# Kernel optimization log

Hardware: AMD Instinct MI355X
Metric: run time of the kernel (lower is better)

Reference implementation:

```python
import jax, jax.numpy as jnp
import numpy as np

B, S, H = 2, 1024, 1024
NH, HD = 16, 64
W = 4  # attention_window / number of cached previous-layer states
LS_INIT = 0.1  # layer_scale_init_value
EPS = 1e-5


def _layernorm(x, scale, bias):
    mu = jnp.mean(x, axis=-1, keepdims=True)
    var = jnp.mean(jnp.square(x - mu), axis=-1, keepdims=True)
    return (x - mu) * jax.lax.rsqrt(var + EPS) * scale + bias


def _rope(x, pos):
    # x: [B, L, NH, HD], pos: [L]
    half = x.shape[-1] // 2
    freq = 1.0 / (10000.0 ** (jnp.arange(half, dtype=x.dtype) / half))
    ang = pos.astype(x.dtype)[:, None] * freq[None, :]           # [L, half]
    cos = jnp.cos(ang)[None, :, None, :]
    sin = jnp.sin(ang)[None, :, None, :]
    x1, x2 = jnp.split(x, 2, axis=-1)
    return jnp.concatenate([x1 * cos - x2 * sin, x1 * sin + x2 * cos], axis=-1)


def setup_inputs() -> dict:
    key = jax.random.key(0)
    ks = jax.random.split(key, 8)
    w_std = 0.02
    return {
        'hidden_states': jax.random.normal(ks[0], (B, S, H), jnp.float32),
        'cache_states': jax.random.normal(ks[1], (W, B, S, H), jnp.float32),
        'ln_scale': jnp.ones((H,), jnp.float32),
        'ln_bias': jnp.zeros((H,), jnp.float32),
        'Wq': jax.random.normal(ks[2], (H, NH * HD), jnp.float32) * w_std,
        'Wk': jax.random.normal(ks[3], (H, NH * HD), jnp.float32) * w_std,
        'Wv': jax.random.normal(ks[4], (H, NH * HD), jnp.float32) * w_std,
        'Wo': jax.random.normal(ks[5], (NH * HD, H), jnp.float32) * w_std,
        'gate_param': jax.random.normal(ks[6], (H,), jnp.float32),
        'layer_scale_param': jnp.full((H,), LS_INIT, jnp.float32),
    }


def reference(hidden_states, cache_states, ln_scale, ln_bias, Wq, Wk, Wv, Wo,
              gate_param, layer_scale_param):
    b, s, h = hidden_states.shape
    w = cache_states.shape[0]

    # pre-norm
    normed = _layernorm(hidden_states, ln_scale, ln_bias)

    # gather cached previous-layer states (already normalized in cache) and
    # stack them with the current layer along the KV axis: [B, (W+1)*S, H]
    prev_flat = jnp.transpose(cache_states, (1, 0, 2, 3)).reshape(b, w * s, h)
    kv_in = jnp.concatenate([prev_flat, normed], axis=1)

    q = (normed @ Wq).reshape(b, s, NH, HD)
    k = (kv_in @ Wk).reshape(b, (w + 1) * s, NH, HD)
    v = (kv_in @ Wv).reshape(b, (w + 1) * s, NH, HD)

    pos_q = jnp.arange(s)
    pos_k = jnp.tile(jnp.arange(s), w + 1)  # same token positions per layer
    q = _rope(q, pos_q)
    k = _rope(k, pos_k)

    scale = 1.0 / jnp.sqrt(jnp.asarray(HD, hidden_states.dtype))
    scores = jnp.einsum('bqhd,bkhd->bhqk', q, k) * scale   # [B,NH,S,(W+1)S]
    attn = jax.nn.softmax(scores, axis=-1)
    ctx = jnp.einsum('bhqk,bkhd->bqhd', attn, v).reshape(b, s, NH * HD)
    attn_out = ctx @ Wo

    # gated residual with layer scale; cross_layer = most recent cached state
    cross_layer = cache_states[-1]
    g = jax.nn.sigmoid(gate_param)
    combined = g * attn_out + (1.0 - g) * cross_layer
    output = hidden_states + layer_scale_param * combined

    # LRU cache update: evict oldest slot, append normalized new state
    new_state = _layernorm(output, ln_scale, ln_bias)
    new_cache = jnp.concatenate([cache_states[1:], new_state[None]], axis=0)
    return output, new_cache
```

## Files before the change

### kernel.cpp

```cpp
#include <hip/hip_runtime.h>
#include <math.h>

typedef unsigned short u16;

constexpr int cB = 2;
constexpr int cS = 1024;
constexpr int cH = 1024;
constexpr int cNH = 16;
constexpr int cHD = 64;
constexpr int cW = 4;
constexpr int cL = (cW + 1) * cS;
constexpr float cEPS = 1e-5f;

typedef short s16x8 __attribute__((ext_vector_type(8)));
typedef float f32x4 __attribute__((ext_vector_type(4)));

__device__ __forceinline__ float u2f(u16 u) {
  union { unsigned int i; float f; } x; x.i = ((unsigned int)u) << 16; return x.f;
}
__device__ __forceinline__ u16 f2u(float f) {
  union { float f; unsigned int i; } x; x.f = f;
  unsigned int i = x.i;
  i += 0x7fffu + ((i >> 16) & 1u);
  return (u16)(i >> 16);
}
__device__ __forceinline__ u16 f2u_rt(float f) {
  union { __bf16 b; u16 u; } c; c.b = (__bf16)f; return c.u;
}
__device__ __forceinline__ s16x8 ld_frag(const u16* p) {
  uint4 v = *(const uint4*)p;
  union { uint4 u; s16x8 s; } c; c.u = v; return c.s;
}
__device__ __forceinline__ s16x8 u4_frag(uint4 v) {
  union { uint4 u; s16x8 s; } c; c.u = v; return c.s;
}
__device__ __forceinline__ void gl_lds16(const u16* g, u16* l) {
  __builtin_amdgcn_global_load_lds(
      (const __attribute__((address_space(1))) unsigned int*)g,
      (__attribute__((address_space(3))) unsigned int*)l, 16, 0, 0);
}
template <int CTRL>
__device__ __forceinline__ float dpp_fmax(float x) {
  union { float f; int i; } a, r;
  a.f = x;
  r.i = __builtin_amdgcn_update_dpp(a.i, a.i, CTRL, 0xF, 0xF, true);
  return fmaxf(x, r.f);
}

__global__ __launch_bounds__(256) void ln_f32(
    const float* __restrict__ src, float* __restrict__ dst,
    const float* __restrict__ scale, const float* __restrict__ bias)
{
  int r = blockIdx.x;
  int t = threadIdx.x;
  const float* sp = src + (size_t)r * cH;
  float4 x = ((const float4*)sp)[t];
  float s1 = x.x + x.y + x.z + x.w;
  float s2 = x.x * x.x + x.y * x.y + x.z * x.z + x.w * x.w;
  #pragma unroll
  for (int off = 32; off > 0; off >>= 1) {
    s1 += __shfl_down(s1, off);
    s2 += __shfl_down(s2, off);
  }
  __shared__ float w1[4], w2[4];
  __shared__ float stat[2];
  int wid = t >> 6, lid = t & 63;
  if (lid == 0) { w1[wid] = s1; w2[wid] = s2; }
  __syncthreads();
  if (t == 0) {
    float a = w1[0] + w1[1] + w1[2] + w1[3];
    float b = w2[0] + w2[1] + w2[2] + w2[3];
    float mu = a * (1.f / cH);
    float var = b * (1.f / cH) - mu * mu;
    if (var < 0.f) var = 0.f;
    stat[0] = mu; stat[1] = rsqrtf(var + cEPS);
  }
  __syncthreads();
  float mu = stat[0], rs = stat[1];
  int h0 = t * 4;
  float4 sc = *(const float4*)(scale + h0);
  float4 bi = *(const float4*)(bias + h0);
  float4 o;
  o.x = (x.x - mu) * rs * sc.x + bi.x;
  o.y = (x.y - mu) * rs * sc.y + bi.y;
  o.z = (x.z - mu) * rs * sc.z + bi.z;
  o.w = (x.w - mu) * rs * sc.w + bi.w;
  *(float4*)(dst + (size_t)r * cH + h0) = o;
}

__global__ __launch_bounds__(256) void ln_bf16(
    const float* __restrict__ src, u16* __restrict__ kvin,
    const float* __restrict__ scale, const float* __restrict__ bias)
{
  int r = blockIdx.x;
  int t = threadIdx.x;
  const float* sp = src + (size_t)r * cH;
  float4 x = ((const float4*)sp)[t];
  float s1 = x.x + x.y + x.z + x.w;
  float s2 = x.x * x.x + x.y * x.y + x.z * x.z + x.w * x.w;
  #pragma unroll
  for (int off = 32; off > 0; off >>= 1) {
    s1 += __shfl_down(s1, off);
    s2 += __shfl_down(s2, off);
  }
  __shared__ float w1[4], w2[4];
  __shared__ float stat[2];
  int wid = t >> 6, lid = t & 63;
  if (lid == 0) { w1[wid] = s1; w2[wid] = s2; }
  __syncthreads();
  if (t == 0) {
    float a = w1[0] + w1[1] + w1[2] + w1[3];
    float b = w2[0] + w2[1] + w2[2] + w2[3];
    float mu = a * (1.f / cH);
    float var = b * (1.f / cH) - mu * mu;
    if (var < 0.f) var = 0.f;
    stat[0] = mu; stat[1] = rsqrtf(var + cEPS);
  }
  __syncthreads();
  float mu = stat[0], rs = stat[1];
  int h0 = t * 4;
  float4 sc = *(const float4*)(scale + h0);
  float4 bi = *(const float4*)(bias + h0);
  int b = r >> 10, s = r & (cS - 1);
  u16* dp = kvin + ((size_t)(b * cL + cW * cS + s)) * cH + h0;
  ushort4 o; u16* op = (u16*)&o;
  op[0] = f2u((x.x - mu) * rs * sc.x + bi.x);
  op[1] = f2u((x.y - mu) * rs * sc.y + bi.y);
  op[2] = f2u((x.z - mu) * rs * sc.z + bi.z);
  op[3] = f2u((x.w - mu) * rs * sc.w + bi.w);
  *(ushort4*)dp = o;
}

__global__ __launch_bounds__(256) void cache2kv(const float* __restrict__ cache,
                                                u16* __restrict__ kvin) {
  int blk = blockIdx.x;
  int b = blk >> 12, w = (blk >> 10) & 3, s = blk & 1023;
  const float* src = cache + ((size_t)((w * cB + b) * cS + s)) * cH;
  u16* dst = kvin + ((size_t)(b * cL + w * cS + s)) * cH;
  int t = threadIdx.x;
  float4 v = *(const float4*)(src + t * 4);
  ushort4 o; u16* op = (u16*)&o;
  op[0] = f2u(v.x); op[1] = f2u(v.y); op[2] = f2u(v.z); op[3] = f2u(v.w);
  *(ushort4*)(dst + t * 4) = o;
}

__global__ __launch_bounds__(256) void wtrans(
    const float* __restrict__ W0, const float* __restrict__ W1,
    const float* __restrict__ W2, const float* __restrict__ W3,
    u16* __restrict__ Wt)
{
  __shared__ float tile[32][33];
  int mat = blockIdx.z;
  const float* W = (mat == 0) ? W0 : (mat == 1) ? W1 : (mat == 2) ? W2 : W3;
  u16* out = Wt + (size_t)mat * cH * cH;
  int k0 = blockIdx.y * 32, n0 = blockIdx.x * 32;
  int t = threadIdx.x;
  int r = t >> 3, c = (t & 7) * 4;
  float4 v = *(const float4*)(W + (size_t)(k0 + r) * cH + n0 + c);
  tile[r][c] = v.x; tile[r][c + 1] = v.y; tile[r][c + 2] = v.z; tile[r][c + 3] = v.w;
  __syncthreads();
  ushort4 o; u16* op = (u16*)&o;
  #pragma unroll
  for (int j = 0; j < 4; j++) op[j] = f2u(tile[c + j][r]);
  *(ushort4*)(out + (size_t)(n0 + r) * cH + k0 + c) = o;
}

constexpr int GBM = 128, GBN = 128, TLD = 136;

__global__ __launch_bounds__(256) void mgemm(
    const u16* __restrict__ A, const u16* __restrict__ Wt,
    int a_rpb, int a_base, int a_stride,
    int c_rpb, int mode,
    u16* __restrict__ Cb, u16* __restrict__ Cb2,
    const float* __restrict__ hidden, const float* __restrict__ cachefull,
    const float* __restrict__ gate, const float* __restrict__ lsc,
    float* __restrict__ outp)
{
  __shared__ __align__(16) u16 smem[128 * TLD];

  int t = threadIdx.x;
  int m0 = blockIdx.y * GBM, n0 = blockIdx.x * GBN;
  int wave = t >> 6, lane = t & 63, l15 = lane & 15, quad = lane >> 4;
  int wm = (wave >> 1) * 64, wn = (wave & 1) * 64;

  int sr = t >> 2, sk = (t & 3) * 8;
  int rg0 = m0 + sr, rg1 = rg0 + 64;
  int ab0 = rg0 / a_rpb, ab1 = rg1 / a_rpb;
  const u16* arow0 = A + (size_t)(ab0 * a_stride + a_base + (rg0 - ab0 * a_rpb)) * cH + sk;
  const u16* arow1 = A + (size_t)(ab1 * a_stride + a_base + (rg1 - ab1 * a_rpb)) * cH + sk;
  const u16* wrow0 = Wt + (size_t)(n0 + sr) * cH + sk;
  const u16* wrow1 = Wt + (size_t)(n0 + sr + 64) * cH + sk;

  u16* As0 = smem;
  u16* Bs0 = smem + 8192;
  int wofs = wave * 512;

  f32x4 acc[4][4] = {};

  gl_lds16(arow0, As0 + wofs);
  gl_lds16(arow1, As0 + 2048 + wofs);
  gl_lds16(wrow0, Bs0 + wofs);
  gl_lds16(wrow1, Bs0 + 2048 + wofs);

  constexpr int NK = cH / 32;
  for (int kt = 0; kt < NK; kt++) {
    int cur = kt & 1;
    asm volatile("" ::: "memory");
    __builtin_amdgcn_s_barrier();
    asm volatile("" ::: "memory");
    int nk = kt + 1; if (nk == NK) nk = 0;
    int nko = nk * 32;
    u16* Abn = As0 + (cur ^ 1) * 4096;
    u16* Bbn = Bs0 + (cur ^ 1) * 4096;
    gl_lds16(arow0 + nko, Abn + wofs);
    gl_lds16(arow1 + nko, Abn + 2048 + wofs);
    gl_lds16(wrow0 + nko, Bbn + wofs);
    gl_lds16(wrow1 + nko, Bbn + 2048 + wofs);
    asm volatile("s_waitcnt vmcnt(4)" ::: "memory");
    __builtin_amdgcn_s_barrier();
    asm volatile("" ::: "memory");
    const u16* Ab = As0 + cur * 4096;
    const u16* Bb = Bs0 + cur * 4096;
    s16x8 af[4], bf[4];
    #pragma unroll
    for (int mt = 0; mt < 4; mt++)
      af[mt] = *(const s16x8*)&Ab[(wm + mt * 16 + l15) * 32 + quad * 8];
    #pragma unroll
    for (int nt = 0; nt < 4; nt++)
      bf[nt] = *(const s16x8*)&Bb[(wn + nt * 16 + l15) * 32 + quad * 8];
    #pragma unroll
    for (int mt = 0; mt < 4; mt++)
      #pragma unroll
      for (int nt = 0; nt < 4; nt++)
        acc[mt][nt] = __builtin_amdgcn_mfma_f32_16x16x32_bf16(af[mt], bf[nt], acc[mt][nt], 0, 0, 0);
  }

  int mode_eff = mode;
  u16* Cout = Cb;
  int nbase = n0;
  if (mode == 5) {
    if (n0 < cH) { mode_eff = 1; }
    else { mode_eff = 3; Cout = Cb2; nbase = n0 - cH; }
  }

  if (mode_eff == 1) {
    #pragma unroll
    for (int mt = 0; mt < 4; mt++)
      #pragma unroll
      for (int i = 0; i < 4; i++) {
        int rg = m0 + wm + mt * 16 + quad * 4 + i;
        int bo = rg / c_rpb, lo = rg - bo * c_rpb;
        #pragma unroll
        for (int nt = 0; nt < 4; nt++) {
          int n = nbase + wn + nt * 16 + l15;
          int h = n >> 6, d = n & 63;
          Cout[(((size_t)(bo * cNH + h) * c_rpb + lo) * cHD) + d] = f2u(acc[mt][nt][i]);
        }
      }
  } else if (mode_eff == 3) {
    u16* t2 = smem;
    asm volatile("s_waitcnt vmcnt(0)" ::: "memory");
    __syncthreads();
    #pragma unroll
    for (int mt = 0; mt < 4; mt++)
      #pragma unroll
      for (int nt = 0; nt < 4; nt++) {
        ushort4 o; u16* op = (u16*)&o;
        #pragma unroll
        for (int i = 0; i < 4; i++) op[i] = f2u(acc[mt][nt][i]);
        *(ushort4*)&t2[(size_t)(wn + nt * 16 + l15) * TLD + wm + mt * 16 + quad * 4] = o;
      }
    __syncthreads();
    int n_l = t >> 1, mh = (t & 1) * 64;
    int bo = m0 / c_rpb;
    int lo = m0 - bo * c_rpb + mh;
    int n = nbase + n_l, h = n >> 6, d = n & 63;
    u16* dst = Cout + ((size_t)(bo * cNH + h) * cHD + d) * (size_t)c_rpb + lo;
    #pragma unroll
    for (int j = 0; j < 8; j++)
      *(uint4*)(dst + j * 8) = *(const uint4*)&t2[(size_t)n_l * TLD + mh + j * 8];
  } else {
    float gv[4], lv[4];
    #pragma unroll
    for (int nt = 0; nt < 4; nt++) {
      int n = n0 + wn + nt * 16 + l15;
      gv[nt] = 1.f / (1.f + __expf(-gate[n]));
      lv[nt] = lsc[n];
    }
    #pragma unroll
    for (int mt = 0; mt < 4; mt++)
      #pragma unroll
      for (int i = 0; i < 4; i++) {
        int rg = m0 + wm + mt * 16 + quad * 4 + i;
        size_t rbase = (size_t)rg * cH;
        #pragma unroll
        for (int nt = 0; nt < 4; nt++) {
          int n = n0 + wn + nt * 16 + l15;
          float hid = hidden[rbase + n];
          float cr = cachefull[(size_t)3 * cB * cS * cH + rbase + n];
          outp[rbase + n] = hid + lv[nt] * (gv[nt] * acc[mt][nt][i] + (1.f - gv[nt]) * cr);
        }
      }
  }
}

__global__ __launch_bounds__(256) void rope_b16(u16* __restrict__ X, int rows) {
  size_t idx = (size_t)blockIdx.x * 256 + threadIdx.x;
  int d = (int)(idx & 31);
  size_t rest = idx >> 5;
  int row = (int)(rest % rows);
  size_t bh = rest / rows;
  u16* xp = X + (bh * rows + row) * cHD;
  int pos = row & (cS - 1);
  float freq = exp2f(-(float)d * (13.287712379549449f / 32.f));
  float ang = (float)pos * freq;
  float sn, cs;
  sincosf(ang, &sn, &cs);
  float x1 = u2f(xp[d]), x2 = u2f(xp[d + 32]);
  xp[d] = f2u(x1 * cs - x2 * sn);
  xp[d + 32] = f2u(x1 * sn + x2 * cs);
}

constexpr int ACK = 64;
constexpr int PLD = 72;
constexpr int KSPLIT = 4;
constexpr int KS = cL / KSPLIT;
constexpr int NIT = KS / ACK;
constexpr int NRB = cB * cNH * cS;

__global__ __launch_bounds__(256, 4) void attn_mfma(
    const u16* __restrict__ Q, const u16* __restrict__ K, const u16* __restrict__ Vt,
    float* __restrict__ o0, float* __restrict__ o1,
    float* __restrict__ o2, float* __restrict__ o3,
    float* __restrict__ mlbuf)
{
  __shared__ __align__(16) u16 kls[2][ACK * cHD];
  __shared__ u16 pbuf[4][16 * PLD];

  int t = threadIdx.x;
  int wave = t >> 6, lane = t & 63;
  int l15 = lane & 15, quad = lane >> 4;
  int qt = blockIdx.x, h = blockIdx.y;
  int bz = blockIdx.z;
  int b = bz & (cB - 1), split = bz >> 1;
  int q0 = qt * 64 + wave * 16;
  int kbase = split * KS;

  const u16* qp = Q + ((size_t)(b * cNH + h) * cS + q0) * cHD;
  const char* kp = (const char*)(K + ((size_t)(b * cNH + h) * cL + kbase) * cHD);
  const u16* vp = Vt + (size_t)(b * cNH + h) * cHD * cL + kbase;
  u16* pw = pbuf[wave];

  int P0 = wave * 1024 + lane * 16;
  int P1 = P0 + 4096;
  int s0 = P0 ^ (((P0 >> 7) & 7) << 4);
  int s1 = P1 ^ (((P1 >> 7) & 7) << 4);
  int fsw0 = (quad * 16) ^ ((l15 & 7) << 4);
  int fsw1 = (64 + quad * 16) ^ ((l15 & 7) << 4);

  s16x8 qf0 = ld_frag(qp + (size_t)l15 * cHD + quad * 8);
  s16x8 qf1 = ld_frag(qp + (size_t)l15 * cHD + 32 + quad * 8);

  gl_lds16((const u16*)(kp + s0), (u16*)((char*)&kls[0][0] + wave * 1024));
  gl_lds16((const u16*)(kp + s1), (u16*)((char*)&kls[0][0] + 4096 + wave * 1024));

  f32x4 oacc[4] = {};
  float mrow[4], lrow[4];
  #pragma unroll
  for (int i = 0; i < 4; i++) { mrow[i] = -1e30f; lrow[i] = 0.f; }

  constexpr float SCL = 0.125f * 1.4426950408889634f;

  for (int kt = 0; kt < NIT; kt++) {
    int cur = kt & 1;
    uint4 vreg[8];
    #pragma unroll
    for (int dt = 0; dt < 4; dt++) {
      const u16* vr = vp + (size_t)(dt * 16 + l15) * cL + kt * ACK;
      vreg[2 * dt]     = *(const uint4*)(vr + quad * 8);
      vreg[2 * dt + 1] = *(const uint4*)(vr + 32 + quad * 8);
    }
    asm volatile("" ::: "memory");
    __builtin_amdgcn_s_barrier();
    asm volatile("" ::: "memory");
    int nk = kt + 1; if (nk == NIT) nk = 0;
    const char* kn = kp + (size_t)nk * (ACK * cHD * 2);
    gl_lds16((const u16*)(kn + s0), (u16*)((char*)&kls[cur ^ 1][0] + wave * 1024));
    gl_lds16((const u16*)(kn + s1), (u16*)((char*)&kls[cur ^ 1][0] + 4096 + wave * 1024));
    asm volatile("s_waitcnt vmcnt(10)" ::: "memory");
    __builtin_amdgcn_s_barrier();
    asm volatile("" ::: "memory");
    const char* kc = (const char*)&kls[cur][0];
    f32x4 sc[4];
    __builtin_amdgcn_s_setprio(1);
    #pragma unroll
    for (int nt = 0; nt < 4; nt++) {
      s16x8 kf0 = *(const s16x8*)(kc + (nt * 16 + l15) * 128 + fsw0);
      s16x8 kf1 = *(const s16x8*)(kc + (nt * 16 + l15) * 128 + fsw1);
      f32x4 a = {};
      a = __builtin_amdgcn_mfma_f32_16x16x32_bf16(qf0, kf0, a, 0, 0, 0);
      a = __builtin_amdgcn_mfma_f32_16x16x32_bf16(qf1, kf1, a, 0, 0, 0);
      sc[nt] = a * SCL;
    }
    __builtin_amdgcn_s_setprio(0);
    float mx[4];
    #pragma unroll
    for (int i = 0; i < 4; i++)
      mx[i] = fmaxf(fmaxf(sc[0][i], sc[1][i]), fmaxf(sc[2][i], sc[3][i]));
    #pragma unroll
    for (int i = 0; i < 4; i++) {
      mx[i] = dpp_fmax<0xB1>(mx[i]);
      mx[i] = dpp_fmax<0x4E>(mx[i]);
      mx[i] = dpp_fmax<0x141>(mx[i]);
      mx[i] = dpp_fmax<0x140>(mx[i]);
    }
    bool need = (mx[0] > mrow[0]) | (mx[1] > mrow[1]) |
                (mx[2] > mrow[2]) | (mx[3] > mrow[3]);
    if (__any(need)) {
      float alpha[4];
      #pragma unroll
      for (int i = 0; i < 4; i++) {
        float mn = fmaxf(mrow[i], mx[i]);
        alpha[i] = exp2f(mrow[i] - mn);
        mrow[i] = mn;
        lrow[i] *= alpha[i];
      }
      #pragma unroll
      for (int dt = 0; dt < 4; dt++)
        #pragma unroll
        for (int i = 0; i < 4; i++) oacc[dt][i] *= alpha[i];
    }
    float ps[4] = {};
    #pragma unroll
    for (int nt = 0; nt < 4; nt++)
      #pragma unroll
      for (int i = 0; i < 4; i++) {
        float p = exp2f(sc[nt][i] - mrow[i]);
        ps[i] += p;
        pw[(quad * 4 + i) * PLD + nt * 16 + l15] = f2u_rt(p);
      }
    #pragma unroll
    for (int i = 0; i < 4; i++) lrow[i] += ps[i];
    s16x8 pf0 = *(const s16x8*)&pw[l15 * PLD + quad * 8];
    s16x8 pf1 = *(const s16x8*)&pw[l15 * PLD + 32 + quad * 8];
    __builtin_amdgcn_s_setprio(1);
    #pragma unroll
    for (int dt = 0; dt < 4; dt++) {
      oacc[dt] = __builtin_amdgcn_mfma_f32_16x16x32_bf16(pf0, u4_frag(vreg[2 * dt]), oacc[dt], 0, 0, 0);
      oacc[dt] = __builtin_amdgcn_mfma_f32_16x16x32_bf16(pf1, u4_frag(vreg[2 * dt + 1]), oacc[dt], 0, 0, 0);
    }
    __builtin_amdgcn_s_setprio(0);
  }
  #pragma unroll
  for (int off = 1; off < 16; off <<= 1)
    #pragma unroll
    for (int i = 0; i < 4; i++) lrow[i] += __shfl_xor(lrow[i], off);
  float* ob = (split == 0) ? o0 : (split == 1) ? o1 : (split == 2) ? o2 : o3;
  #pragma unroll
  for (int i = 0; i < 4; i++) {
    int q = q0 + quad * 4 + i;
    size_t Rl = (size_t)(b * cNH + h) * cS + q;
    float* orow = ob + Rl * cHD;
    #pragma unroll
    for (int dt = 0; dt < 4; dt++)
      orow[dt * 16 + l15] = oacc[dt][i];
    if (l15 == 0) {
      mlbuf[((size_t)split * NRB + Rl) * 2] = mrow[i];
      mlbuf[((size_t)split * NRB + Rl) * 2 + 1] = lrow[i];
    }
  }
}

__global__ __launch_bounds__(256) void attn_merge(
    const float* __restrict__ o0, const float* __restrict__ o1,
    const float* __restrict__ o2, const float* __restrict__ o3,
    const float* __restrict__ mlbuf, u16* __restrict__ ctx)
{
  int t = threadIdx.x;
  int R = blockIdx.x * 4 + (t >> 6);
  int d = t & 63;
  float ms[KSPLIT], ls[KSPLIT];
  float m = -1e30f;
  #pragma unroll
  for (int s = 0; s < KSPLIT; s++) {
    ms[s] = mlbuf[((size_t)s * NRB + R) * 2];
    ls[s] = mlbuf[((size_t)s * NRB + R) * 2 + 1];
    m = fmaxf(m, ms[s]);
  }
  const float* ops[KSPLIT] = {o0, o1, o2, o3};
  float num = 0.f, den = 0.f;
  #pragma unroll
  for (int s = 0; s < KSPLIT; s++) {
    float a = exp2f(ms[s] - m);
    num += ops[s][(size_t)R * cHD + d] * a;
    den += ls[s] * a;
  }
  float val = num / den;
  int q = R & (cS - 1), h = (R >> 10) & 15, b = R >> 14;
  ctx[((size_t)b * cS + q) * cH + h * cHD + d] = f2u(val);
}

extern "C" void kernel_launch(void* const* d_in, const int* in_sizes, int n_in,
                              void* d_out, int out_size, void* d_ws, size_t ws_size,
                              hipStream_t stream)
{
  const float* hidden = (const float*)d_in[0];
  const float* cache  = (const float*)d_in[1];
  const float* ln_s   = (const float*)d_in[2];
  const float* ln_b   = (const float*)d_in[3];
  const float* Wq     = (const float*)d_in[4];
  const float* Wk     = (const float*)d_in[5];
  const float* Wv     = (const float*)d_in[6];
  const float* Wo     = (const float*)d_in[7];
  const float* gate   = (const float*)d_in[8];
  const float* lsc    = (const float*)d_in[9];
  float* outp = (float*)d_out;

  u16* kvin = (u16*)d_ws;
  u16* vt   = kvin + (size_t)cB * cL * cH;
  float* opart = (float*)(vt + (size_t)cB * cL * cH);
  float* o0 = opart;
  float* o1 = opart + (size_t)cB * cNH * cS * cHD;
  u16* qb  = kvin;
  u16* ctx = kvin + (size_t)2 * 1024 * 1024;
  float* o2 = (float*)(kvin + (size_t)4 * 1024 * 1024);
  float* mlbuf = (float*)(kvin + (size_t)8 * 1024 * 1024);
  float* o3 = outp;
  u16* kb = (u16*)(outp + (size_t)cB * cS * cH);
  u16* Wt = (u16*)(outp + (size_t)(1 + 3) * cB * cS * cH);
  u16* Wt_q = Wt;
  u16* Wt_k = Wt + (size_t)cH * cH;
  u16* Wt_v = Wt + (size_t)2 * cH * cH;
  u16* Wt_o = Wt + (size_t)3 * cH * cH;

  wtrans<<<dim3(32, 32, 4), 256, 0, stream>>>(Wq, Wk, Wv, Wo, Wt);
  cache2kv<<<cB * cW * cS, 256, 0, stream>>>(cache, kvin);
  ln_bf16<<<cB * cS, 256, 0, stream>>>(hidden, kvin, ln_s, ln_b);

  mgemm<<<dim3(16, (cB * cL) / GBM), 256, 0, stream>>>(
      kvin, Wt_k, cL, 0, cL, cL, 5, kb, vt, nullptr, nullptr, nullptr, nullptr, nullptr);
  mgemm<<<dim3(8, (cB * cS) / GBM), 256, 0, stream>>>(
      kvin, Wt_q, cS, cW * cS, cL, cS, 1, qb, nullptr, nullptr, nullptr, nullptr, nullptr, nullptr);

  rope_b16<<<(cB * cNH * cS * 32) / 256, 256, 0, stream>>>(qb, cS);
  rope_b16<<<(cB * cNH * cL * 32) / 256, 256, 0, stream>>>(kb, cL);

  attn_mfma<<<dim3(cS / 64, cNH, cB * KSPLIT), 256, 0, stream>>>(
      qb, kb, vt, o0, o1, o2, o3, mlbuf);
  attn_merge<<<(cB * cNH * cS) / 4, 256, 0, stream>>>(o0, o1, o2, o3, mlbuf, ctx);

  mgemm<<<dim3(8, (cB * cS) / GBM), 256, 0, stream>>>(
      ctx, Wt_o, cB * cS, 0, cB * cS, cB * cS, 2, nullptr, nullptr,
      hidden, cache, gate, lsc, outp);

  hipMemcpyAsync(outp + (size_t)cB * cS * cH, cache + (size_t)cB * cS * cH,
                 (size_t)(cW - 1) * cB * cS * cH * sizeof(float),
                 hipMemcpyDeviceToDevice, stream);
  ln_f32<<<cB * cS, 256, 0, stream>>>(outp, outp + (size_t)cW * cB * cS * cH, ln_s, ln_b);
}
```

Measured before the change: 432.4 us.

## Process two query tiles per wave in attention to reuse K/V loads

Each wave now handles two 16-row query tiles (128 queries per block instead of 64), sharing every K fragment read from LDS and every V register load across both tiles. The grid along the query axis is halved. This is meant to halve K/V global and LDS traffic per query, at the cost of doubled accumulator and softmax state registers, fewer blocks, and possibly lower occupancy. The V loads are also split into two halves to spread out register pressure, and the vmcnt wait is adjusted to match.

```diff
diff --git a/kernel.cpp b/kernel.cpp
--- a/kernel.cpp
+++ b/kernel.cpp
@@ -335,7 +335,7 @@
     float* __restrict__ mlbuf)
 {
   __shared__ __align__(16) u16 kls[2][ACK * cHD];
-  __shared__ u16 pbuf[4][16 * PLD];
+  __shared__ u16 pbuf[4][2][16 * PLD];
 
   int t = threadIdx.x;
   int wave = t >> 6, lane = t & 63;
@@ -343,13 +343,16 @@
   int qt = blockIdx.x, h = blockIdx.y;
   int bz = blockIdx.z;
   int b = bz & (cB - 1), split = bz >> 1;
-  int q0 = qt * 64 + wave * 16;
+  int q0a = qt * 128 + wave * 16;
+  int q0b = q0a + 64;
   int kbase = split * KS;
 
-  const u16* qp = Q + ((size_t)(b * cNH + h) * cS + q0) * cHD;
+  const u16* qpa = Q + ((size_t)(b * cNH + h) * cS + q0a) * cHD;
+  const u16* qpb = qpa + (size_t)64 * cHD;
   const char* kp = (const char*)(K + ((size_t)(b * cNH + h) * cL + kbase) * cHD);
   const u16* vp = Vt + (size_t)(b * cNH + h) * cHD * cL + kbase;
-  u16* pw = pbuf[wave];
+  u16* pwA = &pbuf[wave][0][0];
+  u16* pwB = &pbuf[wave][1][0];
 
   int P0 = wave * 1024 + lane * 16;
   int P1 = P0 + 4096;
@@ -358,27 +361,32 @@
   int fsw0 = (quad * 16) ^ ((l15 & 7) << 4);
   int fsw1 = (64 + quad * 16) ^ ((l15 & 7) << 4);
 
-  s16x8 qf0 = ld_frag(qp + (size_t)l15 * cHD + quad * 8);
-  s16x8 qf1 = ld_frag(qp + (size_t)l15 * cHD + 32 + quad * 8);
+  s16x8 qa0 = ld_frag(qpa + (size_t)l15 * cHD + quad * 8);
+  s16x8 qa1 = ld_frag(qpa + (size_t)l15 * cHD + 32 + quad * 8);
+  s16x8 qb0f = ld_frag(qpb + (size_t)l15 * cHD + quad * 8);
+  s16x8 qb1f = ld_frag(qpb + (size_t)l15 * cHD + 32 + quad * 8);
 
   gl_lds16((const u16*)(kp + s0), (u16*)((char*)&kls[0][0] + wave * 1024));
   gl_lds16((const u16*)(kp + s1), (u16*)((char*)&kls[0][0] + 4096 + wave * 1024));
 
-  f32x4 oacc[4] = {};
-  float mrow[4], lrow[4];
-  #pragma unroll
-  for (int i = 0; i < 4; i++) { mrow[i] = -1e30f; lrow[i] = 0.f; }
+  f32x4 oacc[2][4] = {};
+  float mrowA[4], lrowA[4], mrowB[4], lrowB[4];
+  #pragma unroll
+  for (int i = 0; i < 4; i++) {
+    mrowA[i] = -1e30f; lrowA[i] = 0.f;
+    mrowB[i] = -1e30f; lrowB[i] = 0.f;
+  }
 
   constexpr float SCL = 0.125f * 1.4426950408889634f;
 
   for (int kt = 0; kt < NIT; kt++) {
     int cur = kt & 1;
-    uint4 vreg[8];
-    #pragma unroll
-    for (int dt = 0; dt < 4; dt++) {
+    uint4 v01[4];
+    #pragma unroll
+    for (int dt = 0; dt < 2; dt++) {
       const u16* vr = vp + (size_t)(dt * 16 + l15) * cL + kt * ACK;
-      vreg[2 * dt]     = *(const uint4*)(vr + quad * 8);
-      vreg[2 * dt + 1] = *(const uint4*)(vr + 32 + quad * 8);
+      v01[2 * dt]     = *(const uint4*)(vr + quad * 8);
+      v01[2 * dt + 1] = *(const uint4*)(vr + 32 + quad * 8);
     }
     asm volatile("" ::: "memory");
     __builtin_amdgcn_s_barrier();
@@ -387,86 +395,149 @@
     const char* kn = kp + (size_t)nk * (ACK * cHD * 2);
     gl_lds16((const u16*)(kn + s0), (u16*)((char*)&kls[cur ^ 1][0] + wave * 1024));
     gl_lds16((const u16*)(kn + s1), (u16*)((char*)&kls[cur ^ 1][0] + 4096 + wave * 1024));
-    asm volatile("s_waitcnt vmcnt(10)" ::: "memory");
+    asm volatile("s_waitcnt vmcnt(6)" ::: "memory");
     __builtin_amdgcn_s_barrier();
     asm volatile("" ::: "memory");
     const char* kc = (const char*)&kls[cur][0];
-    f32x4 sc[4];
+    f32x4 scA[4], scB[4];
     __builtin_amdgcn_s_setprio(1);
     #pragma unroll
     for (int nt = 0; nt < 4; nt++) {
       s16x8 kf0 = *(const s16x8*)(kc + (nt * 16 + l15) * 128 + fsw0);
       s16x8 kf1 = *(const s16x8*)(kc + (nt * 16 + l15) * 128 + fsw1);
       f32x4 a = {};
-      a = __builtin_amdgcn_mfma_f32_16x16x32_bf16(qf0, kf0, a, 0, 0, 0);
-      a = __builtin_amdgcn_mfma_f32_16x16x32_bf16(qf1, kf1, a, 0, 0, 0);
-      sc[nt] = a * SCL;
+      a = __builtin_amdgcn_mfma_f32_16x16x32_bf16(qa0, kf0, a, 0, 0, 0);
+      a = __builtin_amdgcn_mfma_f32_16x16x32_bf16(qa1, kf1, a, 0, 0, 0);
+      scA[nt] = a * SCL;
+      f32x4 c = {};
+      c = __builtin_amdgcn_mfma_f32_16x16x32_bf16(qb0f, kf0, c, 0, 0, 0);
+      c = __builtin_amdgcn_mfma_f32_16x16x32_bf16(qb1f, kf1, c, 0, 0, 0);
+      scB[nt] = c * SCL;
     }
     __builtin_amdgcn_s_setprio(0);
-    float mx[4];
-    #pragma unroll
-    for (int i = 0; i < 4; i++)
-      mx[i] = fmaxf(fmaxf(sc[0][i], sc[1][i]), fmaxf(sc[2][i], sc[3][i]));
+    float mxA[4], mxB[4];
     #pragma unroll
     for (int i = 0; i < 4; i++) {
-      mx[i] = dpp_fmax<0xB1>(mx[i]);
-      mx[i] = dpp_fmax<0x4E>(mx[i]);
-      mx[i] = dpp_fmax<0x141>(mx[i]);
-      mx[i] = dpp_fmax<0x140>(mx[i]);
-    }
-    bool need = (mx[0] > mrow[0]) | (mx[1] > mrow[1]) |
-                (mx[2] > mrow[2]) | (mx[3] > mrow[3]);
-    if (__any(need)) {
+      mxA[i] = fmaxf(fmaxf(scA[0][i], scA[1][i]), fmaxf(scA[2][i], scA[3][i]));
+      mxB[i] = fmaxf(fmaxf(scB[0][i], scB[1][i]), fmaxf(scB[2][i], scB[3][i]));
+    }
+    #pragma unroll
+    for (int i = 0; i < 4; i++) {
+      mxA[i] = dpp_fmax<0xB1>(mxA[i]);  mxB[i] = dpp_fmax<0xB1>(mxB[i]);
+      mxA[i] = dpp_fmax<0x4E>(mxA[i]);  mxB[i] = dpp_fmax<0x4E>(mxB[i]);
+      mxA[i] = dpp_fmax<0x141>(mxA[i]); mxB[i] = dpp_fmax<0x141>(mxB[i]);
+      mxA[i] = dpp_fmax<0x140>(mxA[i]); mxB[i] = dpp_fmax<0x140>(mxB[i]);
+    }
+    bool needA = (mxA[0] > mrowA[0]) | (mxA[1] > mrowA[1]) |
+                 (mxA[2] > mrowA[2]) | (mxA[3] > mrowA[3]);
+    if (__any(needA)) {
       float alpha[4];
       #pragma unroll
       for (int i = 0; i < 4; i++) {
-        float mn = fmaxf(mrow[i], mx[i]);
-        alpha[i] = exp2f(mrow[i] - mn);
-        mrow[i] = mn;
-        lrow[i] *= alpha[i];
+        float mn = fmaxf(mrowA[i], mxA[i]);
+        alpha[i] = exp2f(mrowA[i] - mn);
+        mrowA[i] = mn;
+        lrowA[i] *= alpha[i];
       }
       #pragma unroll
       for (int dt = 0; dt < 4; dt++)
         #pragma unroll
-        for (int i = 0; i < 4; i++) oacc[dt][i] *= alpha[i];
-    }
-    float ps[4] = {};
-    #pragma unroll
-    for (int nt = 0; nt < 4; nt++)
+        for (int i = 0; i < 4; i++) oacc[0][dt][i] *= alpha[i];
+    }
+    bool needB = (mxB[0] > mrowB[0]) | (mxB[1] > mrowB[1]) |
+                 (mxB[2] > mrowB[2]) | (mxB[3] > mrowB[3]);
+    if (__any(needB)) {
+      float alpha[4];
       #pragma unroll
       for (int i = 0; i < 4; i++) {
-        float p = exp2f(sc[nt][i] - mrow[i]);
-        ps[i] += p;
-        pw[(quad * 4 + i) * PLD + nt * 16 + l15] = f2u_rt(p);
+        float mn = fmaxf(mrowB[i], mxB[i]);
+        alpha[i] = exp2f(mrowB[i] - mn);
+        mrowB[i] = mn;
+        lrowB[i] *= alpha[i];
       }
-    #pragma unroll
-    for (int i = 0; i < 4; i++) lrow[i] += ps[i];
-    s16x8 pf0 = *(const s16x8*)&pw[l15 * PLD + quad * 8];
-    s16x8 pf1 = *(const s16x8*)&pw[l15 * PLD + 32 + quad * 8];
+      #pragma unroll
+      for (int dt = 0; dt < 4; dt++)
+        #pragma unroll
+        for (int i = 0; i < 4; i++) oacc[1][dt][i] *= alpha[i];
+    }
+    {
+      float ps[4] = {};
+      #pragma unroll
+      for (int nt = 0; nt < 4; nt++)
+        #pragma unroll
+        for (int i = 0; i < 4; i++) {
+          float p = exp2f(scA[nt][i] - mrowA[i]);
+          ps[i] += p;
+          pwA[(quad * 4 + i) * PLD + nt * 16 + l15] = f2u_rt(p);
+        }
+      #pragma unroll
+      for (int i = 0; i < 4; i++) lrowA[i] += ps[i];
+    }
+    uint4 v23[4];
+    #pragma unroll
+    for (int dt = 2; dt < 4; dt++) {
+      const u16* vr = vp + (size_t)(dt * 16 + l15) * cL + kt * ACK;
+      v23[2 * (dt - 2)]     = *(const uint4*)(vr + quad * 8);
+      v23[2 * (dt - 2) + 1] = *(const uint4*)(vr + 32 + quad * 8);
+    }
+    {
+      float ps[4] = {};
+      #pragma unroll
+      for (int nt = 0; nt < 4; nt++)
+        #pragma unroll
+        for (int i = 0; i < 4; i++) {
+          float p = exp2f(scB[nt][i] - mrowB[i]);
+          ps[i] += p;
+          pwB[(quad * 4 + i) * PLD + nt * 16 + l15] = f2u_rt(p);
+        }
+      #pragma unroll
+      for (int i = 0; i < 4; i++) lrowB[i] += ps[i];
+    }
+    s16x8 pfA0 = *(const s16x8*)&pwA[l15 * PLD + quad * 8];
+    s16x8 pfA1 = *(const s16x8*)&pwA[l15 * PLD + 32 + quad * 8];
+    s16x8 pfB0 = *(const s16x8*)&pwB[l15 * PLD + quad * 8];
+    s16x8 pfB1 = *(const s16x8*)&pwB[l15 * PLD + 32 + quad * 8];
     __builtin_amdgcn_s_setprio(1);
     #pragma unroll
-    for (int dt = 0; dt < 4; dt++) {
-      oacc[dt] = __builtin_amdgcn_mfma_f32_16x16x32_bf16(pf0, u4_frag(vreg[2 * dt]), oacc[dt], 0, 0, 0);
-      oacc[dt] = __builtin_amdgcn_mfma_f32_16x16x32_bf16(pf1, u4_frag(vreg[2 * dt + 1]), oacc[dt], 0, 0, 0);
+    for (int dt = 0; dt < 2; dt++) {
+      oacc[0][dt] = __builtin_amdgcn_mfma_f32_16x16x32_bf16(pfA0, u4_frag(v01[2 * dt]), oacc[0][dt], 0, 0, 0);
+      oacc[0][dt] = __builtin_amdgcn_mfma_f32_16x16x32_bf16(pfA1, u4_frag(v01[2 * dt + 1]), oacc[0][dt], 0, 0, 0);
+      oacc[1][dt] = __builtin_amdgcn_mfma_f32_16x16x32_bf16(pfB0, u4_frag(v01[2 * dt]), oacc[1][dt], 0, 0, 0);
+      oacc[1][dt] = __builtin_amdgcn_mfma_f32_16x16x32_bf16(pfB1, u4_frag(v01[2 * dt + 1]), oacc[1][dt], 0, 0, 0);
+    }
+    #pragma unroll
+    for (int dt = 2; dt < 4; dt++) {
+      int vi = 2 * (dt - 2);
+      oacc[0][dt] = __builtin_amdgcn_mfma_f32_16x16x32_bf16(pfA0, u4_frag(v23[vi]), oacc[0][dt], 0, 0, 0);
+      oacc[0][dt] = __builtin_amdgcn_mfma_f32_16x16x32_bf16(pfA1, u4_frag(v23[vi + 1]), oacc[0][dt], 0, 0, 0);
+      oacc[1][dt] = __builtin_amdgcn_mfma_f32_16x16x32_bf16(pfB0, u4_frag(v23[vi]), oacc[1][dt], 0, 0, 0);
+      oacc[1][dt] = __builtin_amdgcn_mfma_f32_16x16x32_bf16(pfB1, u4_frag(v23[vi + 1]), oacc[1][dt], 0, 0, 0);
     }
     __builtin_amdgcn_s_setprio(0);
   }
   #pragma unroll
   for (int off = 1; off < 16; off <<= 1)
     #pragma unroll
-    for (int i = 0; i < 4; i++) lrow[i] += __shfl_xor(lrow[i], off);
+    for (int i = 0; i < 4; i++) {
+      lrowA[i] += __shfl_xor(lrowA[i], off);
+      lrowB[i] += __shfl_xor(lrowB[i], off);
+    }
   float* ob = (split == 0) ? o0 : (split == 1) ? o1 : (split == 2) ? o2 : o3;
   #pragma unroll
-  for (int i = 0; i < 4; i++) {
-    int q = q0 + quad * 4 + i;
-    size_t Rl = (size_t)(b * cNH + h) * cS + q;
-    float* orow = ob + Rl * cHD;
-    #pragma unroll
-    for (int dt = 0; dt < 4; dt++)
-      orow[dt * 16 + l15] = oacc[dt][i];
-    if (l15 == 0) {
-      mlbuf[((size_t)split * NRB + Rl) * 2] = mrow[i];
-      mlbuf[((size_t)split * NRB + Rl) * 2 + 1] = lrow[i];
+  for (int x = 0; x < 2; x++) {
+    int qbase = x ? q0b : q0a;
+    #pragma unroll
+    for (int i = 0; i < 4; i++) {
+      int q = qbase + quad * 4 + i;
+      size_t Rl = (size_t)(b * cNH + h) * cS + q;
+      float* orow = ob + Rl * cHD;
+      #pragma unroll
+      for (int dt = 0; dt < 4; dt++)
+        orow[dt * 16 + l15] = oacc[x][dt][i];
+      if (l15 == 0) {
+        mlbuf[((size_t)split * NRB + Rl) * 2]     = x ? mrowB[i] : mrowA[i];
+        mlbuf[((size_t)split * NRB + Rl) * 2 + 1] = x ? lrowB[i] : lrowA[i];
+      }
     }
   }
 }
@@ -545,7 +616,7 @@
   rope_b16<<<(cB * cNH * cS * 32) / 256, 256, 0, stream>>>(qb, cS);
   rope_b16<<<(cB * cNH * cL * 32) / 256, 256, 0, stream>>>(kb, cL);
 
-  attn_mfma<<<dim3(cS / 64, cNH, cB * KSPLIT), 256, 0, stream>>>(
+  attn_mfma<<<dim3(cS / 128, cNH, cB * KSPLIT), 256, 0, stream>>>(
       qb, kb, vt, o0, o1, o2, o3, mlbuf);
   attn_merge<<<(cB * cNH * cS) / 4, 256, 0, stream>>>(o0, o1, o2, o3, mlbuf, ctx);
 
```

Measured after the change: 438.8 us. About the same (+1.5%).
